# Performance work log

Measured on AMD Instinct MI355X. Metric: run time of the kernel, lower is better.

## Reference

```python
import jax, jax.numpy as jnp
import numpy as np

DIM = 1152
NUM_HEADS = 16
HEAD_DIM = DIM // NUM_HEADS
EPS = 1e-6
B, N, M = 4, 4096, 512


def setup_inputs() -> dict:
    key = jax.random.key(0)
    ks = jax.random.split(key, 12)
    s = 0.02
    return {
        "x": jax.random.normal(ks[0], (B, N, DIM), dtype=jnp.float32),
        "cond": jax.random.normal(ks[1], (B, M, DIM), dtype=jnp.float32),
        "kv_seqlen": jax.random.randint(ks[2], (B,), 1, M + 1, dtype=jnp.int32),
        "q_w": jax.random.normal(ks[3], (DIM, DIM), dtype=jnp.float32) * s,
        "q_b": jnp.zeros((DIM,), jnp.float32),
        "kv_w": jax.random.normal(ks[4], (DIM, 2 * DIM), dtype=jnp.float32) * s,
        "kv_b": jnp.zeros((2 * DIM,), jnp.float32),
        "proj_w": jax.random.normal(ks[5], (DIM, DIM), dtype=jnp.float32) * s,
        "proj_b": jnp.zeros((DIM,), jnp.float32),
        "qn_w": jnp.ones((HEAD_DIM,), jnp.float32),
        "kn_w": jnp.ones((HEAD_DIM,), jnp.float32),
    }


def _rmsnorm_fp32(t, w):
    # RMSNorm computed in fp32 over head_dim, then cast back
    t32 = t.astype(jnp.float32)
    inv = jax.lax.rsqrt(jnp.mean(t32 * t32, axis=-1, keepdims=True) + EPS)
    return ((t32 * inv) * w.astype(jnp.float32)).astype(t.dtype)


def reference(x, cond, kv_seqlen, q_w, q_b, kv_w, kv_b, proj_w, proj_b, qn_w, kn_w):
    b, n, c = x.shape
    out_dtype = x.dtype
    q = (x @ q_w + q_b).reshape(b, n, NUM_HEADS, HEAD_DIM)           # [B,N,H,D]
    kv = (cond @ kv_w + kv_b).reshape(b, -1, 2, NUM_HEADS, HEAD_DIM)
    k, v = kv[:, :, 0], kv[:, :, 1]                                   # [B,M,H,D]
    q = _rmsnorm_fp32(q, qn_w)
    k = _rmsnorm_fp32(k, kn_w)
    # original casts to bf16 for the attention kernel when out_dtype is fp32
    q16, k16, v16 = q.astype(jnp.bfloat16), k.astype(jnp.bfloat16), v.astype(jnp.bfloat16)
    scale = 1.0 / np.sqrt(HEAD_DIM)
    scores = jnp.einsum("bnhd,bmhd->bhnm", q16, k16,
                        preferred_element_type=jnp.float32) * scale   # [B,H,N,M] fp32
    m = cond.shape[1]
    valid = (jnp.arange(m)[None, :] < kv_seqlen[:, None])             # [B,M] ragged kv mask
    scores = jnp.where(valid[:, None, None, :], scores, -jnp.inf)
    probs = jax.nn.softmax(scores, axis=-1).astype(jnp.bfloat16)
    out = jnp.einsum("bhnm,bmhd->bnhd", probs, v16).reshape(b, n, c)
    out = out.astype(out_dtype)
    return out @ proj_w + proj_b
```

## Files before the change

kernel.cpp:

```cpp
#include <hip/hip_runtime.h>
#include <math.h>

typedef unsigned short ushort_t;
typedef __attribute__((ext_vector_type(4))) float floatx4;
typedef __attribute__((ext_vector_type(8))) short bf16x8;

#define DIMC 1152
#define NHEADS 16
#define HDIM 72

__device__ __forceinline__ ushort_t f2bf(float f) {
  unsigned u = __float_as_uint(f);
  u += 0x7FFFu + ((u >> 16) & 1u);
  return (ushort_t)(u >> 16);
}
__device__ __forceinline__ float bf2f(ushort_t s) {
  return __uint_as_float(((unsigned)s) << 16);
}

__device__ __forceinline__ void gload_lds16(const ushort_t* g, ushort_t* l) {
  __builtin_amdgcn_global_load_lds(
      (const __attribute__((address_space(1))) unsigned int*)(const void*)g,
      (__attribute__((address_space(3))) unsigned int*)(void*)l, 16, 0, 0);
}

__device__ __forceinline__ bf16x8 load_bf16x8(const ushort_t* p) {
  union { bf16x8 v; uint4 u; } t;
  t.u = *(const uint4*)p;
  return t.v;
}

__global__ void cvt_bf16_kernel(const float* __restrict__ src,
                                ushort_t* __restrict__ dst, int n8) {
  int i = blockIdx.x * 256 + threadIdx.x;
  if (i >= n8) return;
  float4 f0 = ((const float4*)src)[2 * (size_t)i];
  float4 f1 = ((const float4*)src)[2 * (size_t)i + 1];
  union { ushort_t s[8]; uint4 u; } t;
  t.s[0] = f2bf(f0.x); t.s[1] = f2bf(f0.y); t.s[2] = f2bf(f0.z); t.s[3] = f2bf(f0.w);
  t.s[4] = f2bf(f1.x); t.s[5] = f2bf(f1.y); t.s[6] = f2bf(f1.z); t.s[7] = f2bf(f1.w);
  ((uint4*)dst)[i] = t.u;
}

__global__ void transpose_w_kernel(const float* __restrict__ W,
                                   ushort_t* __restrict__ Wt, int K, int N) {
  __shared__ ushort_t tile[64 * 80];
  int k0 = blockIdx.x * 64, n0 = blockIdx.y * 64;
  int tid = threadIdx.x;
  int kl = tid >> 4, n4 = tid & 15;
  for (int rr = 0; rr < 4; rr++) {
    int k = kl + rr * 16;
    float4 f = *(const float4*)(W + (size_t)(k0 + k) * N + n0 + n4 * 4);
    tile[(n4 * 4 + 0) * 80 + k] = f2bf(f.x);
    tile[(n4 * 4 + 1) * 80 + k] = f2bf(f.y);
    tile[(n4 * 4 + 2) * 80 + k] = f2bf(f.z);
    tile[(n4 * 4 + 3) * 80 + k] = f2bf(f.w);
  }
  __syncthreads();
  int nl = tid >> 2, kq = tid & 3;
  uint4 v0 = *(const uint4*)(tile + nl * 80 + kq * 16);
  uint4 v1 = *(const uint4*)(tile + nl * 80 + kq * 16 + 8);
  *(uint4*)(Wt + (size_t)(n0 + nl) * K + k0 + kq * 16) = v0;
  *(uint4*)(Wt + (size_t)(n0 + nl) * K + k0 + kq * 16 + 8) = v1;
}

template <bool OUT_F32>
__global__ __launch_bounds__(256, 4) void gemm128_kernel(
    const ushort_t* __restrict__ A0, const ushort_t* __restrict__ Bt0,
    const float* __restrict__ bias0, void* __restrict__ C0,
    int NTn0, int Ncols0,
    const ushort_t* __restrict__ A1, const ushort_t* __restrict__ Bt1,
    const float* __restrict__ bias1, void* __restrict__ C1,
    int NTn1, int Ncols1,
    int nblk0, int Kdim) {
  __shared__ ushort_t S[16384];

  int lin = blockIdx.x;
  int cpx = gridDim.x >> 3;
  int wg = (lin & 7) * cpx + (lin >> 3);

  const ushort_t* Aseg; const ushort_t* Bseg;
  const float* bias; void* Cptr; int NTn, Ncols;
  if (wg < nblk0) {
    Aseg = A0; Bseg = Bt0; bias = bias0; Cptr = C0; NTn = NTn0; Ncols = Ncols0;
  } else {
    wg -= nblk0;
    Aseg = A1; Bseg = Bt1; bias = bias1; Cptr = C1; NTn = NTn1; Ncols = Ncols1;
  }
  int mt = wg / NTn, nt = wg % NTn;
  int m0 = mt * 128, n0 = nt * 128;

  int tid = threadIdx.x;
  int wid = tid >> 6, lane = tid & 63, quad = lane >> 4, l16 = lane & 15;
  int wr = wid >> 1, wc = wid & 1;
  const int qoff = (quad * 8) ^ ((l16 & 8) << 1);

  const int srow = tid >> 2;
  const int scol = ((tid & 3) * 8) ^ ((tid & 32) ? 16 : 0);
  const ushort_t* Abase = Aseg + (size_t)m0 * Kdim;
  const ushort_t* Bbase = Bseg + (size_t)n0 * Kdim;

  auto stageA = [&](int t) {
    const ushort_t* src = Abase + (size_t)srow * Kdim + t * 32 + scol;
    ushort_t* dst = S + (t & 1) * 8192 + (tid >> 6) * 512;
    gload_lds16(src, dst);
    gload_lds16(src + (size_t)64 * Kdim, dst + 2048);
  };
  auto stageB = [&](int t) {
    const ushort_t* src = Bbase + (size_t)srow * Kdim + t * 32 + scol;
    ushort_t* dst = S + (t & 1) * 8192 + 4096 + (tid >> 6) * 512;
    gload_lds16(src, dst);
    gload_lds16(src + (size_t)64 * Kdim, dst + 2048);
  };

  floatx4 zero = {0.f, 0.f, 0.f, 0.f};
  floatx4 acc[4][4];
#pragma unroll
  for (int i = 0; i < 4; i++)
#pragma unroll
    for (int j = 0; j < 4; j++) acc[i][j] = zero;

  int NT = Kdim >> 5;

  stageA(0); stageB(0); stageB(1);
  asm volatile("s_waitcnt vmcnt(2)" ::: "memory");
  __builtin_amdgcn_s_barrier();

  for (int t = 0; t < NT; ++t) {
    const int base = (t & 1) * 8192;
    const int arow = base + (wr * 64 + l16) * 32 + qoff;
    const int brow = base + 4096 + (wc * 64 + l16) * 32 + qoff;

    bf16x8 bfr[4], a01[2];
#pragma unroll
    for (int c = 0; c < 4; c++)
      bfr[c] = *(const bf16x8*)(S + brow + c * 512);
    a01[0] = *(const bf16x8*)(S + arow);
    a01[1] = *(const bf16x8*)(S + arow + 512);
    if (t + 1 < NT) stageA(t + 1);
    __builtin_amdgcn_s_barrier();
    asm volatile("s_waitcnt lgkmcnt(0)" ::: "memory");
    __builtin_amdgcn_sched_barrier(0);
    __builtin_amdgcn_s_setprio(1);
#pragma unroll
    for (int c = 0; c < 4; c++) {
      acc[0][c] = __builtin_amdgcn_mfma_f32_16x16x32_bf16(a01[0], bfr[c], acc[0][c], 0, 0, 0);
      acc[1][c] = __builtin_amdgcn_mfma_f32_16x16x32_bf16(a01[1], bfr[c], acc[1][c], 0, 0, 0);
    }
    __builtin_amdgcn_s_setprio(0);
    __builtin_amdgcn_s_barrier();

    bf16x8 a23[2];
    a23[0] = *(const bf16x8*)(S + arow + 1024);
    a23[1] = *(const bf16x8*)(S + arow + 1536);
    if (t + 2 < NT) stageB(t + 2);
    __builtin_amdgcn_s_barrier();
    asm volatile("s_waitcnt lgkmcnt(0)" ::: "memory");
    __builtin_amdgcn_sched_barrier(0);
    __builtin_amdgcn_s_setprio(1);
#pragma unroll
    for (int c = 0; c < 4; c++) {
      acc[2][c] = __builtin_amdgcn_mfma_f32_16x16x32_bf16(a23[0], bfr[c], acc[2][c], 0, 0, 0);
      acc[3][c] = __builtin_amdgcn_mfma_f32_16x16x32_bf16(a23[1], bfr[c], acc[3][c], 0, 0, 0);
    }
    __builtin_amdgcn_s_setprio(0);
    if (t < NT - 2)
      asm volatile("s_waitcnt vmcnt(2)" ::: "memory");
    else
      asm volatile("s_waitcnt vmcnt(0)" ::: "memory");
    __builtin_amdgcn_s_barrier();
  }

  float bv[4];
#pragma unroll
  for (int c = 0; c < 4; c++) bv[c] = bias[n0 + wc * 64 + c * 16 + l16];
#pragma unroll
  for (int mf = 0; mf < 4; mf++)
#pragma unroll
    for (int c = 0; c < 4; c++)
#pragma unroll
      for (int r = 0; r < 4; r++) {
        int row = m0 + wr * 64 + mf * 16 + quad * 4 + r;
        int col = n0 + wc * 64 + c * 16 + l16;
        float v = acc[mf][c][r] + bv[c];
        if constexpr (OUT_F32)
          ((float*)Cptr)[(size_t)row * Ncols + col] = v;
        else
          ((ushort_t*)Cptr)[(size_t)row * Ncols + col] = f2bf(v);
      }
}

__global__ void rmsnorm_heads_kernel(ushort_t* __restrict__ p,
                                     const float* __restrict__ w,
                                     int rowstride) {
  int gw = blockIdx.x * 4 + (threadIdx.x >> 6);
  int lane = threadIdx.x & 63;
  int row = gw >> 4, h = gw & 15;
  ushort_t* base = p + (size_t)row * rowstride + h * HDIM;
  float v0 = bf2f(base[lane]);
  float v1 = (lane < 8) ? bf2f(base[64 + lane]) : 0.f;
  float ss = v0 * v0 + v1 * v1;
  for (int off = 1; off < 64; off <<= 1) ss += __shfl_xor(ss, off);
  float inv = rsqrtf(ss / 72.0f + 1e-6f);
  base[lane] = f2bf(v0 * inv * w[lane]);
  if (lane < 8) base[64 + lane] = f2bf(v1 * inv * w[64 + lane]);
}

__global__ void vtrans_kernel(const ushort_t* __restrict__ kv16,
                              ushort_t* __restrict__ vT) {
  int gw = blockIdx.x * 4 + (threadIdx.x >> 6);
  int lane = threadIdx.x & 63;
  int d = gw % 80;
  int bh = gw / 80;
  int b = bh >> 4, h = bh & 15;
  ushort_t* dst = vT + (size_t)gw * 512;
  if (d < HDIM) {
    const ushort_t* src = kv16 + (size_t)b * 512 * 2304 + DIMC + h * HDIM + d;
    for (int m = lane; m < 512; m += 64) dst[m] = src[(size_t)m * 2304];
  } else {
    ushort_t fill = (d == HDIM) ? (ushort_t)0x3F80 : (ushort_t)0;
    for (int m = lane; m < 512; m += 64) dst[m] = fill;
  }
}

__global__ __launch_bounds__(256, 4) void attn_kernel(
    const ushort_t* __restrict__ q16, const ushort_t* __restrict__ kv16,
    const ushort_t* __restrict__ vT, const int* __restrict__ seqlens,
    const float* __restrict__ qn_w, ushort_t* __restrict__ att) {
  __shared__ ushort_t KV[22 * 512];
  __shared__ ushort_t Ps[4][32 * 64];
  int b = blockIdx.z, h = blockIdx.y, n0 = blockIdx.x * 128;
  int tid = threadIdx.x, wid = tid >> 6, lane = tid & 63;
  int quad = lane >> 4, l16 = lane & 15;
  int seqlen = seqlens[b];
  const float qscale = 0.11785113019775793f * 1.44269504088896f;

  ushort_t* Pw = &Ps[wid][0];

  bf16x8 qf[2][3];
  float ssq[2] = {0.f, 0.f};
  for (int rb = 0; rb < 2; rb++)
    for (int ks = 0; ks < 3; ks++) {
      if (ks == 2 && quad > 0) {
        qf[rb][ks] = (bf16x8){0, 0, 0, 0, 0, 0, 0, 0};
      } else {
        size_t off = ((size_t)(b * 4096 + n0 + wid * 32 + rb * 16 + l16)) * DIMC +
                     h * HDIM + ks * 32 + quad * 8;
        qf[rb][ks] = load_bf16x8(q16 + off);
        union { bf16x8 v; ushort_t s[8]; } e;
        e.v = qf[rb][ks];
        for (int j = 0; j < 8; j++) {
          float x = bf2f(e.s[j]);
          ssq[rb] += x * x;
        }
      }
    }
  for (int rb = 0; rb < 2; rb++) {
    ssq[rb] += __shfl_xor(ssq[rb], 16);
    ssq[rb] += __shfl_xor(ssq[rb], 32);
  }
  for (int rb = 0; rb < 2; rb++) {
    float inv = rsqrtf(ssq[rb] / 72.0f + 1e-6f) * qscale;
    for (int ks = 0; ks < 3; ks++) {
      if (ks == 2 && quad > 0) continue;
      float4 w0 = *(const float4*)(qn_w + ks * 32 + quad * 8);
      float4 w1 = *(const float4*)(qn_w + ks * 32 + quad * 8 + 4);
      union { bf16x8 v; ushort_t s[8]; } e;
      e.v = qf[rb][ks];
      e.s[0] = f2bf(bf2f(e.s[0]) * inv * w0.x);
      e.s[1] = f2bf(bf2f(e.s[1]) * inv * w0.y);
      e.s[2] = f2bf(bf2f(e.s[2]) * inv * w0.z);
      e.s[3] = f2bf(bf2f(e.s[3]) * inv * w0.w);
      e.s[4] = f2bf(bf2f(e.s[4]) * inv * w1.x);
      e.s[5] = f2bf(bf2f(e.s[5]) * inv * w1.y);
      e.s[6] = f2bf(bf2f(e.s[6]) * inv * w1.z);
      e.s[7] = f2bf(bf2f(e.s[7]) * inv * w1.w);
      qf[rb][ks] = e.v;
    }
  }

  floatx4 zero = {0.f, 0.f, 0.f, 0.f};
  floatx4 of[2][5];
  for (int rb = 0; rb < 2; rb++)
    for (int nf = 0; nf < 5; nf++) of[rb][nf] = zero;

  const size_t kvrow = (size_t)b * 512;
  const size_t vbase = (size_t)((b * 16 + h) * 80) * 512;

  int ntiles = (seqlen + 63) >> 6;
  for (int mt = 0; mt < ntiles; mt++) {
    int m0 = mt * 64;

    __syncthreads();
    for (int id = wid; id < 22; id += 4) {
      const ushort_t* src;
      if (id < 12) {
        int c = (id * 11) >> 5;
        int ks = id - c * 3;
        src = kv16 + (size_t)(kvrow + m0 + c * 16 + l16) * 2304 + h * HDIM +
              ks * 32 + quad * 8;
      } else {
        int v = id - 12;
        int nf = v >> 1, ks = v & 1;
        src = vT + (vbase + (size_t)(nf * 16 + l16) * 512) + m0 + ks * 32 + quad * 8;
      }
      gload_lds16(src, KV + id * 512);
    }
    __syncthreads();

    floatx4 sf[2][4];
    for (int rb = 0; rb < 2; rb++)
      for (int c = 0; c < 4; c++) sf[rb][c] = zero;
    for (int c = 0; c < 4; c++)
      for (int ks = 0; ks < 3; ks++) {
        bf16x8 kf = *(const bf16x8*)(KV + (c * 3 + ks) * 512 + lane * 8);
        for (int rb = 0; rb < 2; rb++)
          sf[rb][c] = __builtin_amdgcn_mfma_f32_16x16x32_bf16(qf[rb][ks], kf, sf[rb][c], 0, 0, 0);
      }

    for (int rb = 0; rb < 2; rb++)
      for (int c = 0; c < 4; c++) {
        bool valid = (m0 + c * 16 + l16) < seqlen;
        int col = (c * 16 + l16) ^ (quad * 16);
        int rowb = rb * 16 + quad * 4;
        for (int r = 0; r < 4; r++) {
          float pp = valid ? __builtin_amdgcn_exp2f(sf[rb][c][r]) : 0.f;
          Pw[(rowb + r) * 64 + col] = f2bf(pp);
        }
      }

    for (int ks = 0; ks < 2; ks++) {
      bf16x8 pf[2];
      int g = ((ks * 2 + (quad >> 1)) * 16 + (quad & 1) * 8) ^ (((l16 >> 2) & 3) * 16);
      for (int rb = 0; rb < 2; rb++)
        pf[rb] = *(const bf16x8*)(Pw + (rb * 16 + l16) * 64 + g);
      for (int nf = 0; nf < 5; nf++) {
        bf16x8 vf = *(const bf16x8*)(KV + (12 + nf * 2 + ks) * 512 + lane * 8);
        for (int rb = 0; rb < 2; rb++)
          of[rb][nf] = __builtin_amdgcn_mfma_f32_16x16x32_bf16(pf[rb], vf, of[rb][nf], 0, 0, 0);
      }
    }
  }

  for (int rb = 0; rb < 2; rb++) {
    float invl[4];
    for (int r = 0; r < 4; r++) {
      float lsum = __shfl(of[rb][4][r], (lane & 48) | 8);
      invl[r] = 1.0f / lsum;
    }
    for (int nf = 0; nf < 5; nf++) {
      int d = nf * 16 + l16;
      if (d < HDIM) {
        for (int r = 0; r < 4; r++) {
          size_t o = ((size_t)(b * 4096 + n0 + wid * 32 + rb * 16 + quad * 4 + r)) * DIMC +
                     h * HDIM + d;
          att[o] = f2bf(of[rb][nf][r] * invl[r]);
        }
      }
    }
  }
}

extern "C" void kernel_launch(void* const* d_in, const int* in_sizes, int n_in,
                              void* d_out, int out_size, void* d_ws, size_t ws_size,
                              hipStream_t stream) {
  const float* x      = (const float*)d_in[0];
  const float* cond   = (const float*)d_in[1];
  const int*   seqlen = (const int*)d_in[2];
  const float* q_w    = (const float*)d_in[3];
  const float* q_b    = (const float*)d_in[4];
  const float* kv_w   = (const float*)d_in[5];
  const float* kv_b   = (const float*)d_in[6];
  const float* proj_w = (const float*)d_in[7];
  const float* proj_b = (const float*)d_in[8];
  const float* qn_w   = (const float*)d_in[9];
  const float* kn_w   = (const float*)d_in[10];
  float* out = (float*)d_out;

  char* ws = (char*)d_ws;
  size_t o = 0;
  ushort_t* qwT    = (ushort_t*)(ws + o); o += (size_t)1152 * 1152 * 2;
  ushort_t* kvwT   = (ushort_t*)(ws + o); o += (size_t)2304 * 1152 * 2;
  ushort_t* pwT    = (ushort_t*)(ws + o); o += (size_t)1152 * 1152 * 2;
  ushort_t* q16    = (ushort_t*)(ws + o); o += (size_t)16384 * 1152 * 2;
  ushort_t* kv16   = (ushort_t*)(ws + o); o += (size_t)2048 * 2304 * 2;
  ushort_t* vT     = (ushort_t*)(ws + o); o += (size_t)64 * 80 * 512 * 2;
  ushort_t* att    = (ushort_t*)(ws + o); o += (size_t)16384 * 1152 * 2;
  ushort_t* x16    = (ushort_t*)(ws + o); o += (size_t)16384 * 1152 * 2;
  ushort_t* cond16 = (ushort_t*)(ws + o); o += (size_t)2048 * 1152 * 2;

  dim3 blk(256);

  cvt_bf16_kernel<<<dim3((16384 * 1152 / 8 + 255) / 256), blk, 0, stream>>>(
      x, x16, 16384 * 1152 / 8);
  cvt_bf16_kernel<<<dim3((2048 * 1152 / 8 + 255) / 256), blk, 0, stream>>>(
      cond, cond16, 2048 * 1152 / 8);

  transpose_w_kernel<<<dim3(1152 / 64, 1152 / 64), blk, 0, stream>>>(q_w, qwT, 1152, 1152);
  transpose_w_kernel<<<dim3(1152 / 64, 2304 / 64), blk, 0, stream>>>(kv_w, kvwT, 1152, 2304);
  transpose_w_kernel<<<dim3(1152 / 64, 1152 / 64), blk, 0, stream>>>(proj_w, pwT, 1152, 1152);

  gemm128_kernel<false><<<dim3(1152 + 288), blk, 0, stream>>>(
      x16, qwT, q_b, q16, 9, 1152,
      cond16, kvwT, kv_b, kv16, 18, 2304,
      1152, 1152);

  rmsnorm_heads_kernel<<<dim3(2048 * 16 / 4), blk, 0, stream>>>(kv16, kn_w, 2304);

  vtrans_kernel<<<dim3(64 * 80 / 4), blk, 0, stream>>>(kv16, vT);

  attn_kernel<<<dim3(32, 16, 4), blk, 0, stream>>>(q16, kv16, vT, seqlen, qn_w, att);

  gemm128_kernel<true><<<dim3(1152), blk, 0, stream>>>(
      att, pwT, proj_b, out, 9, 1152,
      att, pwT, proj_b, out, 9, 1152,
      1152, 1152);
}
```

Baseline: 385.3 us.

## Triple-buffer GEMM LDS pipeline and tile V transpose through shared memory

The GEMM kernel moves from double to triple buffering in LDS. Both A and B tiles are prefetched two K-steps ahead, with the vmcnt waits adjusted to match, to hide more global-load latency. This costs more LDS per block, so launch bounds drop from 4 to 3 blocks per CU. Separately, the V transpose kernel now stages a 64-row tile in shared memory and writes packed 8-byte vectors, replacing the strided scalar global reads.

```diff
diff --git a/kernel.cpp b/kernel.cpp
--- a/kernel.cpp
+++ b/kernel.cpp
@@ -65,7 +65,7 @@
 }
 
 template <bool OUT_F32>
-__global__ __launch_bounds__(256, 4) void gemm128_kernel(
+__global__ __launch_bounds__(256, 3) void gemm128_kernel(
     const ushort_t* __restrict__ A0, const ushort_t* __restrict__ Bt0,
     const float* __restrict__ bias0, void* __restrict__ C0,
     int NTn0, int Ncols0,
@@ -73,7 +73,7 @@
     const float* __restrict__ bias1, void* __restrict__ C1,
     int NTn1, int Ncols1,
     int nblk0, int Kdim) {
-  __shared__ ushort_t S[16384];
+  __shared__ ushort_t S[24576];
 
   int lin = blockIdx.x;
   int cpx = gridDim.x >> 3;
@@ -100,15 +100,15 @@
   const ushort_t* Abase = Aseg + (size_t)m0 * Kdim;
   const ushort_t* Bbase = Bseg + (size_t)n0 * Kdim;
 
-  auto stageA = [&](int t) {
+  auto stageA = [&](int t, int buf) {
     const ushort_t* src = Abase + (size_t)srow * Kdim + t * 32 + scol;
-    ushort_t* dst = S + (t & 1) * 8192 + (tid >> 6) * 512;
+    ushort_t* dst = S + buf * 8192 + (tid >> 6) * 512;
     gload_lds16(src, dst);
     gload_lds16(src + (size_t)64 * Kdim, dst + 2048);
   };
-  auto stageB = [&](int t) {
+  auto stageB = [&](int t, int buf) {
     const ushort_t* src = Bbase + (size_t)srow * Kdim + t * 32 + scol;
-    ushort_t* dst = S + (t & 1) * 8192 + 4096 + (tid >> 6) * 512;
+    ushort_t* dst = S + buf * 8192 + 4096 + (tid >> 6) * 512;
     gload_lds16(src, dst);
     gload_lds16(src + (size_t)64 * Kdim, dst + 2048);
   };
@@ -122,12 +122,15 @@
 
   int NT = Kdim >> 5;
 
-  stageA(0); stageB(0); stageB(1);
-  asm volatile("s_waitcnt vmcnt(2)" ::: "memory");
+  stageA(0, 0); stageB(0, 0);
+  stageA(1, 1); stageB(1, 1);
+  asm volatile("s_waitcnt vmcnt(4)" ::: "memory");
   __builtin_amdgcn_s_barrier();
 
+  int cur = 0;
   for (int t = 0; t < NT; ++t) {
-    const int base = (t & 1) * 8192;
+    int nx2 = cur + 2; if (nx2 >= 3) nx2 -= 3;
+    const int base = cur * 8192;
     const int arow = base + (wr * 64 + l16) * 32 + qoff;
     const int brow = base + 4096 + (wc * 64 + l16) * 32 + qoff;
 
@@ -137,7 +140,7 @@
       bfr[c] = *(const bf16x8*)(S + brow + c * 512);
     a01[0] = *(const bf16x8*)(S + arow);
     a01[1] = *(const bf16x8*)(S + arow + 512);
-    if (t + 1 < NT) stageA(t + 1);
+    if (t + 2 < NT) stageA(t + 2, nx2);
     __builtin_amdgcn_s_barrier();
     asm volatile("s_waitcnt lgkmcnt(0)" ::: "memory");
     __builtin_amdgcn_sched_barrier(0);
@@ -153,7 +156,7 @@
     bf16x8 a23[2];
     a23[0] = *(const bf16x8*)(S + arow + 1024);
     a23[1] = *(const bf16x8*)(S + arow + 1536);
-    if (t + 2 < NT) stageB(t + 2);
+    if (t + 2 < NT) stageB(t + 2, nx2);
     __builtin_amdgcn_s_barrier();
     asm volatile("s_waitcnt lgkmcnt(0)" ::: "memory");
     __builtin_amdgcn_sched_barrier(0);
@@ -164,11 +167,13 @@
       acc[3][c] = __builtin_amdgcn_mfma_f32_16x16x32_bf16(a23[1], bfr[c], acc[3][c], 0, 0, 0);
     }
     __builtin_amdgcn_s_setprio(0);
-    if (t < NT - 2)
-      asm volatile("s_waitcnt vmcnt(2)" ::: "memory");
+    if (t + 2 < NT)
+      asm volatile("s_waitcnt vmcnt(4)" ::: "memory");
     else
       asm volatile("s_waitcnt vmcnt(0)" ::: "memory");
     __builtin_amdgcn_s_barrier();
+
+    cur = cur + 1; if (cur == 3) cur = 0;
   }
 
   float bv[4];
@@ -208,18 +213,37 @@
 
 __global__ void vtrans_kernel(const ushort_t* __restrict__ kv16,
                               ushort_t* __restrict__ vT) {
-  int gw = blockIdx.x * 4 + (threadIdx.x >> 6);
-  int lane = threadIdx.x & 63;
-  int d = gw % 80;
-  int bh = gw / 80;
-  int b = bh >> 4, h = bh & 15;
-  ushort_t* dst = vT + (size_t)gw * 512;
-  if (d < HDIM) {
-    const ushort_t* src = kv16 + (size_t)b * 512 * 2304 + DIMC + h * HDIM + d;
-    for (int m = lane; m < 512; m += 64) dst[m] = src[(size_t)m * 2304];
-  } else {
-    ushort_t fill = (d == HDIM) ? (ushort_t)0x3F80 : (ushort_t)0;
-    for (int m = lane; m < 512; m += 64) dst[m] = fill;
+  __shared__ ushort_t tile[64 * 84];
+  int b = blockIdx.z, h = blockIdx.y, m0 = blockIdx.x * 64;
+  int tid = threadIdx.x;
+  int row = tid >> 2, sl = tid & 3;
+  const ushort_t* src =
+      kv16 + (size_t)(b * 512 + m0 + row) * 2304 + DIMC + h * HDIM;
+#pragma unroll
+  for (int k = 0; k < 5; k++) {
+    int s = sl + 4 * k;
+    if (s < 18) {
+      uint2 v = *(const uint2*)(src + s * 4);
+      *(uint2*)(tile + row * 84 + s * 4) = v;
+    }
+  }
+  __syncthreads();
+  size_t dbase = (size_t)((b * 16 + h) * 80) * 512 + m0;
+#pragma unroll
+  for (int it = 0; it < 5; it++) {
+    int idx = it * 256 + tid;
+    int d = idx >> 4, mseg = idx & 15;
+    union { ushort_t s[4]; uint2 u; } pk;
+    if (d < HDIM) {
+      pk.s[0] = tile[(mseg * 4 + 0) * 84 + d];
+      pk.s[1] = tile[(mseg * 4 + 1) * 84 + d];
+      pk.s[2] = tile[(mseg * 4 + 2) * 84 + d];
+      pk.s[3] = tile[(mseg * 4 + 3) * 84 + d];
+    } else {
+      ushort_t f = (d == HDIM) ? (ushort_t)0x3F80 : (ushort_t)0;
+      pk.s[0] = pk.s[1] = pk.s[2] = pk.s[3] = f;
+    }
+    *(uint2*)(vT + dbase + (size_t)d * 512 + mseg * 4) = pk.u;
   }
 }
 
@@ -407,7 +431,7 @@
 
   rmsnorm_heads_kernel<<<dim3(2048 * 16 / 4), blk, 0, stream>>>(kv16, kn_w, 2304);
 
-  vtrans_kernel<<<dim3(64 * 80 / 4), blk, 0, stream>>>(kv16, vT);
+  vtrans_kernel<<<dim3(8, 16, 4), blk, 0, stream>>>(kv16, vT);
 
   attn_kernel<<<dim3(32, 16, 4), blk, 0, stream>>>(q16, kv16, vT, seqlen, qn_w, att);
 
```

Measured after the change: 375.8 us. -2.5%, faster.
